# Kernel tuning notes

Measured on AMD Instinct MI355X. Metric: run time of the kernel, lower is better.

## Reference

```python
import jax, jax.numpy as jnp
import numpy as np

N, D, H = 8192, 1024, 256

def setup_inputs() -> dict:
    key = jax.random.key(0)
    ks = jax.random.split(key, 11)
    s = lambda fan_in: 1.0 / np.sqrt(fan_in)
    return {
        "x": jax.random.normal(ks[0], (N, D), dtype=jnp.float32),
        "lin1_w": jax.random.uniform(ks[1], (H, D), jnp.float32, -s(D), s(D)),
        "lin1_b": jax.random.uniform(ks[2], (H,), jnp.float32, -s(D), s(D)),
        "q_w": jax.random.uniform(ks[3], (H, H), jnp.float32, -s(H), s(H)),
        "q_b": jax.random.uniform(ks[4], (H,), jnp.float32, -s(H), s(H)),
        "k_w": jax.random.uniform(ks[5], (H, H), jnp.float32, -s(H), s(H)),
        "k_b": jax.random.uniform(ks[6], (H,), jnp.float32, -s(H), s(H)),
        "v_w": jax.random.uniform(ks[7], (H, H), jnp.float32, -s(H), s(H)),
        "v_b": jax.random.uniform(ks[8], (H,), jnp.float32, -s(H), s(H)),
        "lin2_w": jax.random.uniform(ks[9], (1, H), jnp.float32, -s(H), s(H)),
        "lin2_b": jax.random.uniform(ks[10], (1,), jnp.float32, -s(H), s(H)),
    }

def reference(x, lin1_w, lin1_b, q_w, q_b, k_w, k_b, v_w, v_b, lin2_w, lin2_b):
    h = x @ lin1_w.T + lin1_b                      # [N, H]
    q = h @ q_w.T + q_b                            # [N, H]
    k = h @ k_w.T + k_b                            # [N, H]
    v = h @ v_w.T + v_b                            # [N, H]
    scale = 1.0 / np.sqrt(H).astype(np.float32)
    w = (q @ k.T) * scale                          # [N, N] dense scores
    a = jax.nn.softmax(w, axis=-1)                 # row softmax
    h = h + a @ v                                  # residual
    out = h @ lin2_w.T + lin2_b                    # [N, 1]
    return out.squeeze(-1)                         # [N]
```

## Files before the change

### kernel.cpp

```cpp
#include <hip/hip_runtime.h>
#include <hip/hip_bf16.h>
#include <math.h>

typedef __attribute__((ext_vector_type(4))) float f32x4;
typedef __attribute__((ext_vector_type(8))) short bf16x8;

#define N_TOK 8192
#define D_IN  1024
#define H_DIM 256
#define S_SPLIT 16
#define QSCALE 0.09016844f

static __device__ __forceinline__ float bf2f(unsigned short u) {
  return __uint_as_float(((unsigned)u) << 16);
}
static __device__ __forceinline__ float fast_exp2(float x) {
  float e;
  asm("v_exp_f32 %0, %1" : "=v"(e) : "v"(x));
  return e;
}
static __device__ __forceinline__ void gload_lds16(const void* g, void* l) {
  __builtin_amdgcn_global_load_lds(
      (const __attribute__((address_space(1))) void*)g,
      (__attribute__((address_space(3))) void*)l, 16, 0, 0);
}

__global__ __launch_bounds__(256) void prep_kernel(
    const float* __restrict__ w1, const float* __restrict__ qw,
    const float* __restrict__ kw, const float* __restrict__ vw,
    const float* __restrict__ vb, const float* __restrict__ w2,
    __hip_bfloat16* __restrict__ w1b, __hip_bfloat16* __restrict__ qwb,
    __hip_bfloat16* __restrict__ kwb, float* __restrict__ wv2, float* __restrict__ bv2)
{
  int b = blockIdx.x, tid = threadIdx.x;
  if (b < 384) {
    const float* in; __hip_bfloat16* out; int base;
    if (b < 256)      { in = w1; out = w1b; base = b; }
    else if (b < 320) { in = qw; out = qwb; base = b - 256; }
    else              { in = kw; out = kwb; base = b - 320; }
    int i = base * 1024 + tid * 4;
    float4 v = *reinterpret_cast<const float4*>(in + i);
    union { __hip_bfloat16 h[4]; ushort4 u; } cv;
    cv.h[0] = __float2bfloat16(v.x);
    cv.h[1] = __float2bfloat16(v.y);
    cv.h[2] = __float2bfloat16(v.z);
    cv.h[3] = __float2bfloat16(v.w);
    *reinterpret_cast<ushort4*>(out + i) = cv.u;
    return;
  }
  __shared__ float sw2[256];
  __shared__ float red[256];
  sw2[tid] = w2[tid];
  __syncthreads();
  float a = 0.f;
  #pragma unroll 8
  for (int c = 0; c < 256; ++c) a += vw[c * 256 + tid] * sw2[c];
  wv2[tid] = a;
  red[tid] = vb[tid] * sw2[tid];
  __syncthreads();
  for (int s = 128; s > 0; s >>= 1) {
    if (tid < s) red[tid] += red[tid + s];
    __syncthreads();
  }
  if (tid == 0) bv2[0] = red[0];
}

__global__ __launch_bounds__(512, 4) void lin1_kernel(
    const float* __restrict__ x, const __hip_bfloat16* __restrict__ W1,
    const float* __restrict__ b1, __hip_bfloat16* __restrict__ Ho)
{
  __shared__ __attribute__((aligned(16))) unsigned char lds[2][20480];
  const int tid = threadIdx.x;
  const int w = tid >> 6, l = tid & 63, r16 = l & 15, kg = l >> 4;
  const int wr = w >> 2, wc = w & 3;
  const int rowbase = blockIdx.x * 32;
  const int ch = blockIdx.y;
  const char* Wb = (const char*)W1 + (size_t)ch * 128 * 2048;

  const int xrow = tid >> 4;
  const int xc   = tid & 15;
  const float* xsrc = x + (size_t)(rowbase + xrow) * D_IN + xc * 4;
  const int xdst = xrow * 128 + ((xc * 8) ^ ((xrow & 7) << 4));

  f32x4 acc[2];
  acc[0] = (f32x4){0.f, 0.f, 0.f, 0.f};
  acc[1] = (f32x4){0.f, 0.f, 0.f, 0.f};

  {
    f32x4 xv = *reinterpret_cast<const f32x4*>(xsrc);
    #pragma unroll
    for (int i = 0; i < 2; ++i) {
      int p = i * 8192 + tid * 16;
      int col = p >> 7, bb = p & 127;
      gload_lds16(Wb + (size_t)col * 2048 + (bb ^ ((col & 7) << 4)), &lds[0][4096 + p]);
    }
    union { __hip_bfloat16 h[4]; ushort4 u; } cv;
    cv.h[0] = __float2bfloat16(xv[0]); cv.h[1] = __float2bfloat16(xv[1]);
    cv.h[2] = __float2bfloat16(xv[2]); cv.h[3] = __float2bfloat16(xv[3]);
    *reinterpret_cast<ushort4*>(&lds[0][xdst]) = cv.u;
  }
  __syncthreads();

  const int rsw = (r16 & 7) << 4;
  for (int t = 0; t < 16; ++t) {
    const int cur = t & 1;
    f32x4 xv;
    if (t + 1 < 16) {
      xv = *reinterpret_cast<const f32x4*>(xsrc + (t + 1) * 64);
      const int k0b = (t + 1) * 128;
      #pragma unroll
      for (int i = 0; i < 2; ++i) {
        int p = i * 8192 + tid * 16;
        int col = p >> 7, bb = p & 127;
        gload_lds16(Wb + (size_t)col * 2048 + k0b + (bb ^ ((col & 7) << 4)),
                    &lds[cur ^ 1][4096 + p]);
      }
    }
    const unsigned char* A = &lds[cur][0];
    const unsigned char* W = &lds[cur][4096];
    #pragma unroll
    for (int ks = 0; ks < 2; ++ks) {
      bf16x8 a = *reinterpret_cast<const bf16x8*>(
          A + (wr * 16 + r16) * 128 + ((ks * 64 + kg * 16) ^ rsw));
      #pragma unroll
      for (int c = 0; c < 2; ++c) {
        const int colloc = wc * 32 + c * 16 + r16;
        bf16x8 b = *reinterpret_cast<const bf16x8*>(
            W + colloc * 128 + ((ks * 64 + kg * 16) ^ rsw));
        acc[c] = __builtin_amdgcn_mfma_f32_16x16x32_bf16(a, b, acc[c], 0, 0, 0);
      }
    }
    if (t + 1 < 16) {
      union { __hip_bfloat16 h[4]; ushort4 u; } cv;
      cv.h[0] = __float2bfloat16(xv[0]); cv.h[1] = __float2bfloat16(xv[1]);
      cv.h[2] = __float2bfloat16(xv[2]); cv.h[3] = __float2bfloat16(xv[3]);
      *reinterpret_cast<ushort4*>(&lds[cur ^ 1][xdst]) = cv.u;
    }
    __syncthreads();
  }

  #pragma unroll
  for (int c = 0; c < 2; ++c) {
    int colloc = wc * 32 + c * 16 + r16;
    float bs = b1[ch * 128 + colloc];
    #pragma unroll
    for (int j = 0; j < 4; ++j)
      *reinterpret_cast<__hip_bfloat16*>(
          &lds[0][(wr * 16 + kg * 4 + j) * 256 + colloc * 2]) =
          __float2bfloat16(acc[c][j] + bs);
  }
  __syncthreads();
  {
    int row = tid >> 4, byteo = (tid & 15) * 16;
    uint4 v = *reinterpret_cast<uint4*>(&lds[0][row * 256 + byteo]);
    *reinterpret_cast<uint4*>((char*)Ho + (size_t)(rowbase + row) * 512 + ch * 256 + byteo) = v;
  }
}

__global__ __launch_bounds__(256, 3) void qk_kernel(
    const __hip_bfloat16* __restrict__ Hi,
    const __hip_bfloat16* __restrict__ Wq, const __hip_bfloat16* __restrict__ Wk,
    const float* __restrict__ bq, const float* __restrict__ bk,
    const float* __restrict__ w2, const float* __restrict__ wv2, const float* __restrict__ b2,
    __hip_bfloat16* __restrict__ Qo, __hip_bfloat16* __restrict__ Ko,
    float* __restrict__ hw2, float* __restrict__ vs)
{
  __shared__ __attribute__((aligned(16))) unsigned char lds[8192 + 4096];
  const int tid = threadIdx.x;
  const int w = tid >> 6, l = tid & 63, r16 = l & 15, kg = l >> 4;
  const int rowbase = blockIdx.x * 16;
  const bool isq = (blockIdx.y & 2) == 0;
  const int ch = blockIdx.y & 1;
  const __hip_bfloat16* Wp = isq ? Wq : Wk;
  const int colloc_base = w * 32;
  const int colg_base = ch * 128 + colloc_base;

  #pragma unroll
  for (int i = 0; i < 2; ++i) {
    int p = i * 4096 + tid * 16;
    int row = p >> 9, bb = p & 511;
    gload_lds16((const char*)Hi + (size_t)(rowbase + row) * 512 + (bb ^ ((row & 7) << 4)),
                &lds[p]);
  }

  bf16x8 bfr[8][2];
  #pragma unroll
  for (int ks = 0; ks < 8; ++ks)
    #pragma unroll
    for (int c = 0; c < 2; ++c)
      bfr[ks][c] = *reinterpret_cast<const bf16x8*>(
          Wp + (size_t)(colg_base + c * 16 + r16) * H_DIM + ks * 32 + kg * 8);

  __syncthreads();

  const int rsw = (r16 & 7) << 4;
  bf16x8 afr[8];
  #pragma unroll
  for (int ks = 0; ks < 8; ++ks)
    afr[ks] = *reinterpret_cast<const bf16x8*>(
        &lds[0] + r16 * 512 + ((ks * 64 + kg * 16) ^ rsw));

  f32x4 acc[2];
  acc[0] = (f32x4){0.f, 0.f, 0.f, 0.f};
  acc[1] = (f32x4){0.f, 0.f, 0.f, 0.f};
  #pragma unroll
  for (int ks = 0; ks < 8; ++ks)
    #pragma unroll
    for (int c = 0; c < 2; ++c)
      acc[c] = __builtin_amdgcn_mfma_f32_16x16x32_bf16(afr[ks], bfr[ks][c], acc[c], 0, 0, 0);

  const float* bp = isq ? bq : bk;
  const float scl = isq ? QSCALE : 1.f;
  #pragma unroll
  for (int c = 0; c < 2; ++c) {
    int colloc = colloc_base + c * 16 + r16;
    float bb = bp[ch * 128 + colloc];
    #pragma unroll
    for (int j = 0; j < 4; ++j)
      *reinterpret_cast<__hip_bfloat16*>(&lds[8192 + (kg * 4 + j) * 256 + colloc * 2]) =
          __float2bfloat16((acc[c][j] + bb) * scl);
  }
  __syncthreads();
  {
    int row = tid >> 4, byteo = (tid & 15) * 16;
    uint4 v = *reinterpret_cast<const uint4*>(&lds[8192 + row * 256 + byteo]);
    char* dst = (char*)(isq ? Qo : Ko) + (size_t)(rowbase + row) * 512 + ch * 256 + byteo;
    *reinterpret_cast<uint4*>(dst) = v;
  }
  if (ch == 0) {
    const float* wsel = isq ? w2 : wv2;
    int row = w * 4 + (l >> 4);
    int c16 = l & 15;
    int rs2 = (row & 7) << 4;
    bf16x8 h0 = *reinterpret_cast<const bf16x8*>(&lds[0] + row * 512 + ((c16 * 32) ^ rs2));
    bf16x8 h1 = *reinterpret_cast<const bf16x8*>(&lds[0] + row * 512 + ((c16 * 32 + 16) ^ rs2));
    float s = 0.f;
    #pragma unroll
    for (int i = 0; i < 8; ++i) s += bf2f((unsigned short)h0[i]) * wsel[c16 * 16 + i];
    #pragma unroll
    for (int i = 0; i < 8; ++i) s += bf2f((unsigned short)h1[i]) * wsel[c16 * 16 + 8 + i];
    #pragma unroll
    for (int off = 1; off < 16; off <<= 1) s += __shfl_xor(s, off);
    if (c16 == 0) {
      if (isq) hw2[rowbase + row] = s + b2[0];
      else     vs[rowbase + row]  = s;
    }
  }
}

#define KVBLK 64
#define KRANGE (N_TOK / S_SPLIT)
__global__ __launch_bounds__(256, 2) void attn_partial_kernel(
    const __hip_bfloat16* __restrict__ Q, const __hip_bfloat16* __restrict__ K,
    const float* __restrict__ vsg, float* __restrict__ pden, float* __restrict__ pacc)
{
  __shared__ __attribute__((aligned(16))) unsigned char ktile[2][KVBLK * 512];
  __shared__ float vs_lds[KRANGE];

  const int tid = threadIdx.x;
  const int w   = tid >> 6;
  const int l   = tid & 63;
  const int r16 = l & 15;
  const int kg  = l >> 4;
  const int split   = blockIdx.y;
  const int mstart  = split * KRANGE;
  const int rowbase = blockIdx.x * 256 + w * 64;

  if (tid < KRANGE / 4)
    *reinterpret_cast<float4*>(vs_lds + tid * 4) =
        *reinterpret_cast<const float4*>(vsg + mstart + tid * 4);

  bf16x8 qf[4][8];
  #pragma unroll
  for (int sub = 0; sub < 4; ++sub) {
    const __hip_bfloat16* qp = Q + (size_t)(rowbase + sub * 16 + r16) * H_DIM + kg * 8;
    #pragma unroll
    for (int kk = 0; kk < 8; ++kk) qf[sub][kk] = *reinterpret_cast<const bf16x8*>(qp + kk * 32);
  }

  const int trow = tid >> 5;
  const int tbsw = ((tid & 31) * 16) ^ ((trow & 7) << 4);
  const char* kbase = (const char*)K + (size_t)(mstart + trow) * 512 + tbsw;
  const int ldst = trow * 512 + (tid & 31) * 16;

  const int rsw = (r16 & 7) << 4;
  const int cb  = kg * 16;

  float den[4][4], acc[4][4];
  #pragma unroll
  for (int sub = 0; sub < 4; ++sub)
    #pragma unroll
    for (int j = 0; j < 4; ++j) { den[sub][j] = 0.f; acc[sub][j] = 0.f; }

  #pragma unroll
  for (int i = 0; i < 8; ++i)
    gload_lds16(kbase + (size_t)(i * 8) * 512, &ktile[0][i * 4096 + ldst]);
  __syncthreads();

  const int NT = KRANGE / KVBLK;
  for (int t = 0; t < NT; ++t) {
    const int cur = t & 1;
    if (t + 1 < NT) {
      #pragma unroll
      for (int i = 0; i < 8; ++i)
        gload_lds16(kbase + (size_t)((t + 1) * KVBLK + i * 8) * 512,
                    &ktile[cur ^ 1][i * 4096 + ldst]);
    }

    const unsigned char* kt = &ktile[cur][0];
    #pragma unroll
    for (int h = 0; h < 2; ++h) {
      f32x4 d[4][2];
      #pragma unroll
      for (int sub = 0; sub < 4; ++sub)
        #pragma unroll
        for (int n = 0; n < 2; ++n) d[sub][n] = (f32x4){0.f, 0.f, 0.f, 0.f};

      __builtin_amdgcn_s_setprio(1);
      #pragma unroll
      for (int n = 0; n < 2; ++n) {
        const int row = h * 32 + n * 16 + r16;
        #pragma unroll
        for (int kk = 0; kk < 8; ++kk) {
          bf16x8 b = *reinterpret_cast<const bf16x8*>(
              kt + row * 512 + ((kk * 64 + cb) ^ rsw));
          d[0][n] = __builtin_amdgcn_mfma_f32_16x16x32_bf16(qf[0][kk], b, d[0][n], 0, 0, 0);
          d[1][n] = __builtin_amdgcn_mfma_f32_16x16x32_bf16(qf[1][kk], b, d[1][n], 0, 0, 0);
          d[2][n] = __builtin_amdgcn_mfma_f32_16x16x32_bf16(qf[2][kk], b, d[2][n], 0, 0, 0);
          d[3][n] = __builtin_amdgcn_mfma_f32_16x16x32_bf16(qf[3][kk], b, d[3][n], 0, 0, 0);
        }
      }
      __builtin_amdgcn_s_setprio(0);

      const float vsm0 = vs_lds[t * KVBLK + h * 32 + r16];
      const float vsm1 = vs_lds[t * KVBLK + h * 32 + 16 + r16];
      #pragma unroll
      for (int sub = 0; sub < 4; ++sub)
        #pragma unroll
        for (int j = 0; j < 4; ++j) {
          float e0 = fast_exp2(d[sub][0][j]);
          float e1 = fast_exp2(d[sub][1][j]);
          den[sub][j] += e0 + e1;
          acc[sub][j] = fmaf(e0, vsm0, fmaf(e1, vsm1, acc[sub][j]));
        }
    }
    __syncthreads();
  }

  #pragma unroll
  for (int sub = 0; sub < 4; ++sub)
    #pragma unroll
    for (int j = 0; j < 4; ++j) {
      #pragma unroll
      for (int off = 1; off < 16; off <<= 1) {
        den[sub][j] += __shfl_xor(den[sub][j], off);
        acc[sub][j] += __shfl_xor(acc[sub][j], off);
      }
    }
  if (r16 == 0) {
    #pragma unroll
    for (int sub = 0; sub < 4; ++sub)
      #pragma unroll
      for (int j = 0; j < 4; ++j) {
        int row = rowbase + sub * 16 + kg * 4 + j;
        pden[split * N_TOK + row] = den[sub][j];
        pacc[split * N_TOK + row] = acc[sub][j];
      }
  }
}

__global__ __launch_bounds__(256) void combine_kernel(
    const float* __restrict__ pden, const float* __restrict__ pacc,
    const float* __restrict__ hw2, const float* __restrict__ bv2, float* __restrict__ out)
{
  int r = blockIdx.x * 256 + threadIdx.x;
  float den = 0.f, acc = 0.f;
  #pragma unroll
  for (int s = 0; s < S_SPLIT; ++s) {
    den += pden[s * N_TOK + r];
    acc += pacc[s * N_TOK + r];
  }
  out[r] = hw2[r] + acc / den + bv2[0];
}

extern "C" void kernel_launch(void* const* d_in, const int* in_sizes, int n_in,
                              void* d_out, int out_size, void* d_ws, size_t ws_size,
                              hipStream_t stream) {
  const float* x      = (const float*)d_in[0];
  const float* lin1_w = (const float*)d_in[1];
  const float* lin1_b = (const float*)d_in[2];
  const float* q_w    = (const float*)d_in[3];
  const float* q_b    = (const float*)d_in[4];
  const float* k_w    = (const float*)d_in[5];
  const float* k_b    = (const float*)d_in[6];
  const float* v_w    = (const float*)d_in[7];
  const float* v_b    = (const float*)d_in[8];
  const float* lin2_w = (const float*)d_in[9];
  const float* lin2_b = (const float*)d_in[10];
  float* out = (float*)d_out;

  char* ws = (char*)d_ws;
  size_t off = 0;
  auto alloc = [&](size_t bytes) {
    char* p = ws + off;
    off += (bytes + 255) & ~(size_t)255;
    return p;
  };
  __hip_bfloat16* w1b = (__hip_bfloat16*)alloc((size_t)H_DIM * D_IN * 2);
  __hip_bfloat16* qwb = (__hip_bfloat16*)alloc((size_t)H_DIM * H_DIM * 2);
  __hip_bfloat16* kwb = (__hip_bfloat16*)alloc((size_t)H_DIM * H_DIM * 2);
  __hip_bfloat16* hb  = (__hip_bfloat16*)alloc((size_t)N_TOK * H_DIM * 2);
  __hip_bfloat16* qb  = (__hip_bfloat16*)alloc((size_t)N_TOK * H_DIM * 2);
  __hip_bfloat16* kb  = (__hip_bfloat16*)alloc((size_t)N_TOK * H_DIM * 2);
  float* hw2  = (float*)alloc((size_t)N_TOK * 4);
  float* vsv  = (float*)alloc((size_t)N_TOK * 4);
  float* wv2  = (float*)alloc((size_t)H_DIM * 4);
  float* bv2  = (float*)alloc(256);
  float* pden = (float*)alloc((size_t)S_SPLIT * N_TOK * 4);
  float* pacc = (float*)alloc((size_t)S_SPLIT * N_TOK * 4);
  (void)ws_size; (void)in_sizes; (void)n_in; (void)out_size;

  prep_kernel<<<385, 256, 0, stream>>>(lin1_w, q_w, k_w, v_w, v_b, lin2_w,
                                       w1b, qwb, kwb, wv2, bv2);

  lin1_kernel<<<dim3(N_TOK / 32, 2), 512, 0, stream>>>(x, w1b, lin1_b, hb);

  qk_kernel<<<dim3(N_TOK / 16, 4), 256, 0, stream>>>(hb, qwb, kwb, q_b, k_b,
                                                     lin2_w, wv2, lin2_b, qb, kb, hw2, vsv);

  attn_partial_kernel<<<dim3(32, S_SPLIT), 256, 0, stream>>>(qb, kb, vsv, pden, pacc);

  combine_kernel<<<N_TOK / 256, 256, 0, stream>>>(pden, pacc, hw2, bv2, out);
}
```

Before: 93.96 us.

## Give each wave its own K tile pipeline and stage v_w through LDS

```diff
diff --git a/kernel.cpp b/kernel.cpp
--- a/kernel.cpp
+++ b/kernel.cpp
@@ -49,20 +49,31 @@
     return;
   }
   __shared__ float sw2[256];
-  __shared__ float red[256];
+  __shared__ __attribute__((aligned(16))) float vch[32 * 256];
   sw2[tid] = w2[tid];
-  __syncthreads();
   float a = 0.f;
-  #pragma unroll 8
-  for (int c = 0; c < 256; ++c) a += vw[c * 256 + tid] * sw2[c];
+  for (int ch = 0; ch < 8; ++ch) {
+    __syncthreads();
+    #pragma unroll
+    for (int i = 0; i < 8; ++i) {
+      int p = i * 1024 + tid * 4;
+      *reinterpret_cast<float4*>(vch + p) =
+          *reinterpret_cast<const float4*>(vw + ch * 8192 + p);
+    }
+    __syncthreads();
+    #pragma unroll
+    for (int c = 0; c < 32; ++c)
+      a = fmaf(vch[c * 256 + tid], sw2[ch * 32 + c], a);
+  }
   wv2[tid] = a;
-  red[tid] = vb[tid] * sw2[tid];
+  __syncthreads();
+  vch[tid] = vb[tid] * sw2[tid];
   __syncthreads();
   for (int s = 128; s > 0; s >>= 1) {
-    if (tid < s) red[tid] += red[tid + s];
+    if (tid < s) vch[tid] += vch[tid + s];
     __syncthreads();
   }
-  if (tid == 0) bv2[0] = red[0];
+  if (tid == 0) bv2[0] = vch[0];
 }
 
 __global__ __launch_bounds__(512, 4) void lin1_kernel(
@@ -248,13 +259,14 @@
   }
 }
 
-#define KVBLK 64
+#define KVW 16
 #define KRANGE (N_TOK / S_SPLIT)
+#define NTW (KRANGE / KVW)
 __global__ __launch_bounds__(256, 2) void attn_partial_kernel(
     const __hip_bfloat16* __restrict__ Q, const __hip_bfloat16* __restrict__ K,
     const float* __restrict__ vsg, float* __restrict__ pden, float* __restrict__ pacc)
 {
-  __shared__ __attribute__((aligned(16))) unsigned char ktile[2][KVBLK * 512];
+  __shared__ __attribute__((aligned(16))) unsigned char ktile[4][2][KVW * 512];
   __shared__ float vs_lds[KRANGE];
 
   const int tid = threadIdx.x;
@@ -278,10 +290,11 @@
     for (int kk = 0; kk < 8; ++kk) qf[sub][kk] = *reinterpret_cast<const bf16x8*>(qp + kk * 32);
   }
 
-  const int trow = tid >> 5;
-  const int tbsw = ((tid & 31) * 16) ^ ((trow & 7) << 4);
-  const char* kbase = (const char*)K + (size_t)(mstart + trow) * 512 + tbsw;
-  const int ldst = trow * 512 + (tid & 31) * 16;
+  const int trow = l >> 5;
+  const int tcol = (l & 31) * 16;
+  const char* kb = (const char*)K + (size_t)mstart * 512;
+  unsigned char* wb0 = &ktile[w][0][0];
+  unsigned char* wb1 = &ktile[w][1][0];
 
   const int rsw = (r16 & 7) << 4;
   const int cb  = kg * 16;
@@ -293,58 +306,52 @@
     for (int j = 0; j < 4; ++j) { den[sub][j] = 0.f; acc[sub][j] = 0.f; }
 
   #pragma unroll
-  for (int i = 0; i < 8; ++i)
-    gload_lds16(kbase + (size_t)(i * 8) * 512, &ktile[0][i * 4096 + ldst]);
-  __syncthreads();
-
-  const int NT = KRANGE / KVBLK;
-  for (int t = 0; t < NT; ++t) {
-    const int cur = t & 1;
-    if (t + 1 < NT) {
-      #pragma unroll
-      for (int i = 0; i < 8; ++i)
-        gload_lds16(kbase + (size_t)((t + 1) * KVBLK + i * 8) * 512,
-                    &ktile[cur ^ 1][i * 4096 + ldst]);
-    }
-
-    const unsigned char* kt = &ktile[cur][0];
-    #pragma unroll
-    for (int h = 0; h < 2; ++h) {
-      f32x4 d[4][2];
-      #pragma unroll
-      for (int sub = 0; sub < 4; ++sub)
-        #pragma unroll
-        for (int n = 0; n < 2; ++n) d[sub][n] = (f32x4){0.f, 0.f, 0.f, 0.f};
-
-      __builtin_amdgcn_s_setprio(1);
-      #pragma unroll
-      for (int n = 0; n < 2; ++n) {
-        const int row = h * 32 + n * 16 + r16;
-        #pragma unroll
-        for (int kk = 0; kk < 8; ++kk) {
-          bf16x8 b = *reinterpret_cast<const bf16x8*>(
-              kt + row * 512 + ((kk * 64 + cb) ^ rsw));
-          d[0][n] = __builtin_amdgcn_mfma_f32_16x16x32_bf16(qf[0][kk], b, d[0][n], 0, 0, 0);
-          d[1][n] = __builtin_amdgcn_mfma_f32_16x16x32_bf16(qf[1][kk], b, d[1][n], 0, 0, 0);
-          d[2][n] = __builtin_amdgcn_mfma_f32_16x16x32_bf16(qf[2][kk], b, d[2][n], 0, 0, 0);
-          d[3][n] = __builtin_amdgcn_mfma_f32_16x16x32_bf16(qf[3][kk], b, d[3][n], 0, 0, 0);
-        }
-      }
-      __builtin_amdgcn_s_setprio(0);
-
-      const float vsm0 = vs_lds[t * KVBLK + h * 32 + r16];
-      const float vsm1 = vs_lds[t * KVBLK + h * 32 + 16 + r16];
-      #pragma unroll
-      for (int sub = 0; sub < 4; ++sub)
-        #pragma unroll
-        for (int j = 0; j < 4; ++j) {
-          float e0 = fast_exp2(d[sub][0][j]);
-          float e1 = fast_exp2(d[sub][1][j]);
-          den[sub][j] += e0 + e1;
-          acc[sub][j] = fmaf(e0, vsm0, fmaf(e1, vsm1, acc[sub][j]));
-        }
-    }
-    __syncthreads();
+  for (int i = 0; i < 8; ++i) {
+    const int rg = i * 2 + trow;
+    gload_lds16(kb + (size_t)rg * 512 + (tcol ^ ((rg & 7) << 4)), wb0 + i * 1024);
+  }
+  __syncthreads();
+
+  for (int t = 0; t < NTW; ++t) {
+    unsigned char* rb = (t & 1) ? wb1 : wb0;
+    unsigned char* pb = (t & 1) ? wb0 : wb1;
+    if (t + 1 < NTW) {
+      const char* kt1 = kb + (size_t)(t + 1) * (KVW * 512);
+      #pragma unroll
+      for (int i = 0; i < 8; ++i) {
+        const int rg = i * 2 + trow;
+        gload_lds16(kt1 + (size_t)rg * 512 + (tcol ^ ((rg & 7) << 4)), pb + i * 1024);
+      }
+      asm volatile("s_waitcnt vmcnt(8)" ::: "memory");
+    } else {
+      asm volatile("s_waitcnt vmcnt(0)" ::: "memory");
+    }
+    __builtin_amdgcn_sched_barrier(0);
+
+    f32x4 d[4];
+    #pragma unroll
+    for (int sub = 0; sub < 4; ++sub) d[sub] = (f32x4){0.f, 0.f, 0.f, 0.f};
+
+    __builtin_amdgcn_s_setprio(1);
+    #pragma unroll
+    for (int kk = 0; kk < 8; ++kk) {
+      bf16x8 b = *reinterpret_cast<const bf16x8*>(rb + r16 * 512 + ((kk * 64 + cb) ^ rsw));
+      d[0] = __builtin_amdgcn_mfma_f32_16x16x32_bf16(qf[0][kk], b, d[0], 0, 0, 0);
+      d[1] = __builtin_amdgcn_mfma_f32_16x16x32_bf16(qf[1][kk], b, d[1], 0, 0, 0);
+      d[2] = __builtin_amdgcn_mfma_f32_16x16x32_bf16(qf[2][kk], b, d[2], 0, 0, 0);
+      d[3] = __builtin_amdgcn_mfma_f32_16x16x32_bf16(qf[3][kk], b, d[3], 0, 0, 0);
+    }
+    __builtin_amdgcn_s_setprio(0);
+
+    const float vsm = vs_lds[t * KVW + r16];
+    #pragma unroll
+    for (int sub = 0; sub < 4; ++sub)
+      #pragma unroll
+      for (int j = 0; j < 4; ++j) {
+        float e = fast_exp2(d[sub][j]);
+        den[sub][j] += e;
+        acc[sub][j] = fmaf(e, vsm, acc[sub][j]);
+      }
   }
 
   #pragma unroll
```

Result: no change. 92.22 us (-1.8%).

## Shrink attention tiles, double grid, use explicit waitcnt barriers; stage v_w in LDS

Applied to the files above, without the earlier changes.

```diff
diff --git a/kernel.cpp b/kernel.cpp
--- a/kernel.cpp
+++ b/kernel.cpp
@@ -49,20 +49,31 @@
     return;
   }
   __shared__ float sw2[256];
-  __shared__ float red[256];
+  __shared__ __attribute__((aligned(16))) float vch[32 * 256];
   sw2[tid] = w2[tid];
-  __syncthreads();
   float a = 0.f;
-  #pragma unroll 8
-  for (int c = 0; c < 256; ++c) a += vw[c * 256 + tid] * sw2[c];
+  for (int ch = 0; ch < 8; ++ch) {
+    __syncthreads();
+    #pragma unroll
+    for (int i = 0; i < 8; ++i) {
+      int p = i * 1024 + tid * 4;
+      *reinterpret_cast<float4*>(vch + p) =
+          *reinterpret_cast<const float4*>(vw + ch * 8192 + p);
+    }
+    __syncthreads();
+    #pragma unroll
+    for (int c = 0; c < 32; ++c)
+      a = fmaf(vch[c * 256 + tid], sw2[ch * 32 + c], a);
+  }
   wv2[tid] = a;
-  red[tid] = vb[tid] * sw2[tid];
+  __syncthreads();
+  vch[tid] = vb[tid] * sw2[tid];
   __syncthreads();
   for (int s = 128; s > 0; s >>= 1) {
-    if (tid < s) red[tid] += red[tid + s];
+    if (tid < s) vch[tid] += vch[tid + s];
     __syncthreads();
   }
-  if (tid == 0) bv2[0] = red[0];
+  if (tid == 0) bv2[0] = vch[0];
 }
 
 __global__ __launch_bounds__(512, 4) void lin1_kernel(
@@ -248,9 +259,10 @@
   }
 }
 
-#define KVBLK 64
+#define KVBLK 32
 #define KRANGE (N_TOK / S_SPLIT)
-__global__ __launch_bounds__(256, 2) void attn_partial_kernel(
+#define NT (KRANGE / KVBLK)
+__global__ __launch_bounds__(256, 3) void attn_partial_kernel(
     const __hip_bfloat16* __restrict__ Q, const __hip_bfloat16* __restrict__ K,
     const float* __restrict__ vsg, float* __restrict__ pden, float* __restrict__ pacc)
 {
@@ -264,91 +276,95 @@
   const int kg  = l >> 4;
   const int split   = blockIdx.y;
   const int mstart  = split * KRANGE;
-  const int rowbase = blockIdx.x * 256 + w * 64;
+  const int rowbase = blockIdx.x * 128 + w * 32;
 
   if (tid < KRANGE / 4)
     *reinterpret_cast<float4*>(vs_lds + tid * 4) =
         *reinterpret_cast<const float4*>(vsg + mstart + tid * 4);
 
-  bf16x8 qf[4][8];
-  #pragma unroll
-  for (int sub = 0; sub < 4; ++sub) {
+  bf16x8 qf[2][8];
+  #pragma unroll
+  for (int sub = 0; sub < 2; ++sub) {
     const __hip_bfloat16* qp = Q + (size_t)(rowbase + sub * 16 + r16) * H_DIM + kg * 8;
     #pragma unroll
     for (int kk = 0; kk < 8; ++kk) qf[sub][kk] = *reinterpret_cast<const bf16x8*>(qp + kk * 32);
   }
 
-  const int trow = tid >> 5;
-  const int tbsw = ((tid & 31) * 16) ^ ((trow & 7) << 4);
-  const char* kbase = (const char*)K + (size_t)(mstart + trow) * 512 + tbsw;
-  const int ldst = trow * 512 + (tid & 31) * 16;
+  const char* kb = (const char*)K + (size_t)mstart * 512;
+  int soff[4];
+  #pragma unroll
+  for (int i = 0; i < 4; ++i) {
+    int p = i * 4096 + tid * 16;
+    int row = p >> 9, bb = p & 511;
+    soff[i] = row * 512 + (bb ^ ((row & 7) << 4));
+  }
 
   const int rsw = (r16 & 7) << 4;
   const int cb  = kg * 16;
 
-  float den[4][4], acc[4][4];
-  #pragma unroll
-  for (int sub = 0; sub < 4; ++sub)
+  float den[2][4], acc[2][4];
+  #pragma unroll
+  for (int sub = 0; sub < 2; ++sub)
     #pragma unroll
     for (int j = 0; j < 4; ++j) { den[sub][j] = 0.f; acc[sub][j] = 0.f; }
 
   #pragma unroll
-  for (int i = 0; i < 8; ++i)
-    gload_lds16(kbase + (size_t)(i * 8) * 512, &ktile[0][i * 4096 + ldst]);
-  __syncthreads();
-
-  const int NT = KRANGE / KVBLK;
+  for (int i = 0; i < 4; ++i)
+    gload_lds16(kb + soff[i], &ktile[0][i * 4096 + tid * 16]);
+  __syncthreads();
+
   for (int t = 0; t < NT; ++t) {
     const int cur = t & 1;
     if (t + 1 < NT) {
-      #pragma unroll
-      for (int i = 0; i < 8; ++i)
-        gload_lds16(kbase + (size_t)((t + 1) * KVBLK + i * 8) * 512,
-                    &ktile[cur ^ 1][i * 4096 + ldst]);
-    }
+      const char* kt1 = kb + (size_t)(t + 1) * (KVBLK * 512);
+      #pragma unroll
+      for (int i = 0; i < 4; ++i)
+        gload_lds16(kt1 + soff[i], &ktile[cur ^ 1][i * 4096 + tid * 16]);
+      asm volatile("s_waitcnt vmcnt(4)" ::: "memory");
+    } else {
+      asm volatile("s_waitcnt vmcnt(0)" ::: "memory");
+    }
+    __builtin_amdgcn_s_barrier();
+    __builtin_amdgcn_sched_barrier(0);
 
     const unsigned char* kt = &ktile[cur][0];
-    #pragma unroll
-    for (int h = 0; h < 2; ++h) {
-      f32x4 d[4][2];
-      #pragma unroll
-      for (int sub = 0; sub < 4; ++sub)
-        #pragma unroll
-        for (int n = 0; n < 2; ++n) d[sub][n] = (f32x4){0.f, 0.f, 0.f, 0.f};
-
-      __builtin_amdgcn_s_setprio(1);
-      #pragma unroll
-      for (int n = 0; n < 2; ++n) {
-        const int row = h * 32 + n * 16 + r16;
-        #pragma unroll
-        for (int kk = 0; kk < 8; ++kk) {
-          bf16x8 b = *reinterpret_cast<const bf16x8*>(
-              kt + row * 512 + ((kk * 64 + cb) ^ rsw));
-          d[0][n] = __builtin_amdgcn_mfma_f32_16x16x32_bf16(qf[0][kk], b, d[0][n], 0, 0, 0);
-          d[1][n] = __builtin_amdgcn_mfma_f32_16x16x32_bf16(qf[1][kk], b, d[1][n], 0, 0, 0);
-          d[2][n] = __builtin_amdgcn_mfma_f32_16x16x32_bf16(qf[2][kk], b, d[2][n], 0, 0, 0);
-          d[3][n] = __builtin_amdgcn_mfma_f32_16x16x32_bf16(qf[3][kk], b, d[3][n], 0, 0, 0);
-        }
-      }
-      __builtin_amdgcn_s_setprio(0);
-
-      const float vsm0 = vs_lds[t * KVBLK + h * 32 + r16];
-      const float vsm1 = vs_lds[t * KVBLK + h * 32 + 16 + r16];
-      #pragma unroll
-      for (int sub = 0; sub < 4; ++sub)
-        #pragma unroll
-        for (int j = 0; j < 4; ++j) {
-          float e0 = fast_exp2(d[sub][0][j]);
-          float e1 = fast_exp2(d[sub][1][j]);
-          den[sub][j] += e0 + e1;
-          acc[sub][j] = fmaf(e0, vsm0, fmaf(e1, vsm1, acc[sub][j]));
-        }
-    }
-    __syncthreads();
-  }
-
-  #pragma unroll
-  for (int sub = 0; sub < 4; ++sub)
+    f32x4 d[2][2];
+    #pragma unroll
+    for (int sub = 0; sub < 2; ++sub)
+      #pragma unroll
+      for (int n = 0; n < 2; ++n) d[sub][n] = (f32x4){0.f, 0.f, 0.f, 0.f};
+
+    __builtin_amdgcn_s_setprio(1);
+    #pragma unroll
+    for (int n = 0; n < 2; ++n) {
+      #pragma unroll
+      for (int kk = 0; kk < 8; ++kk) {
+        bf16x8 b = *reinterpret_cast<const bf16x8*>(
+            kt + (n * 16 + r16) * 512 + ((kk * 64 + cb) ^ rsw));
+        d[0][n] = __builtin_amdgcn_mfma_f32_16x16x32_bf16(qf[0][kk], b, d[0][n], 0, 0, 0);
+        d[1][n] = __builtin_amdgcn_mfma_f32_16x16x32_bf16(qf[1][kk], b, d[1][n], 0, 0, 0);
+      }
+    }
+    __builtin_amdgcn_s_setprio(0);
+
+    const float vsm0 = vs_lds[t * KVBLK + r16];
+    const float vsm1 = vs_lds[t * KVBLK + 16 + r16];
+    #pragma unroll
+    for (int sub = 0; sub < 2; ++sub)
+      #pragma unroll
+      for (int j = 0; j < 4; ++j) {
+        float e0 = fast_exp2(d[sub][0][j]);
+        float e1 = fast_exp2(d[sub][1][j]);
+        den[sub][j] += e0 + e1;
+        acc[sub][j] = fmaf(e0, vsm0, fmaf(e1, vsm1, acc[sub][j]));
+      }
+
+    __builtin_amdgcn_sched_barrier(0);
+    __builtin_amdgcn_s_barrier();
+  }
+
+  #pragma unroll
+  for (int sub = 0; sub < 2; ++sub)
     #pragma unroll
     for (int j = 0; j < 4; ++j) {
       #pragma unroll
@@ -359,7 +375,7 @@
     }
   if (r16 == 0) {
     #pragma unroll
-    for (int sub = 0; sub < 4; ++sub)
+    for (int sub = 0; sub < 2; ++sub)
       #pragma unroll
       for (int j = 0; j < 4; ++j) {
         int row = rowbase + sub * 16 + kg * 4 + j;
@@ -428,7 +444,7 @@
   qk_kernel<<<dim3(N_TOK / 16, 4), 256, 0, stream>>>(hb, qwb, kwb, q_b, k_b,
                                                      lin2_w, wv2, lin2_b, qb, kb, hw2, vsv);
 
-  attn_partial_kernel<<<dim3(32, S_SPLIT), 256, 0, stream>>>(qb, kb, vsv, pden, pacc);
+  attn_partial_kernel<<<dim3(64, S_SPLIT), 256, 0, stream>>>(qb, kb, vsv, pden, pacc);
 
   combine_kernel<<<N_TOK / 256, 256, 0, stream>>>(pden, pacc, hw2, bv2, out);
 }
```

After: 99.48 us. 1.06x slower.

## Fuse lin1 and Q/K projection into one front kernel keeping h in LDS

Applied to the files above, without the earlier changes.

```diff
diff --git a/kernel.cpp b/kernel.cpp
--- a/kernel.cpp
+++ b/kernel.cpp
@@ -49,59 +49,73 @@
     return;
   }
   __shared__ float sw2[256];
-  __shared__ float red[256];
+  __shared__ __attribute__((aligned(16))) float vch[32 * 256];
   sw2[tid] = w2[tid];
+  float a = 0.f;
+  for (int ch = 0; ch < 8; ++ch) {
+    __syncthreads();
+    #pragma unroll
+    for (int i = 0; i < 8; ++i) {
+      int p = i * 1024 + tid * 4;
+      *reinterpret_cast<float4*>(vch + p) =
+          *reinterpret_cast<const float4*>(vw + ch * 8192 + p);
+    }
+    __syncthreads();
+    #pragma unroll
+    for (int c = 0; c < 32; ++c)
+      a = fmaf(vch[c * 256 + tid], sw2[ch * 32 + c], a);
+  }
+  wv2[tid] = a;
   __syncthreads();
-  float a = 0.f;
-  #pragma unroll 8
-  for (int c = 0; c < 256; ++c) a += vw[c * 256 + tid] * sw2[c];
-  wv2[tid] = a;
-  red[tid] = vb[tid] * sw2[tid];
+  vch[tid] = vb[tid] * sw2[tid];
   __syncthreads();
   for (int s = 128; s > 0; s >>= 1) {
-    if (tid < s) red[tid] += red[tid + s];
-    __syncthreads();
-  }
-  if (tid == 0) bv2[0] = red[0];
-}
-
-__global__ __launch_bounds__(512, 4) void lin1_kernel(
+    if (tid < s) vch[tid] += vch[tid + s];
+    __syncthreads();
+  }
+  if (tid == 0) bv2[0] = vch[0];
+}
+
+__global__ __launch_bounds__(512) void front_kernel(
     const float* __restrict__ x, const __hip_bfloat16* __restrict__ W1,
-    const float* __restrict__ b1, __hip_bfloat16* __restrict__ Ho)
+    const __hip_bfloat16* __restrict__ Wq, const __hip_bfloat16* __restrict__ Wk,
+    const float* __restrict__ b1, const float* __restrict__ bq, const float* __restrict__ bk,
+    const float* __restrict__ w2, const float* __restrict__ wv2, const float* __restrict__ b2,
+    __hip_bfloat16* __restrict__ Qo, __hip_bfloat16* __restrict__ Ko,
+    float* __restrict__ hw2, float* __restrict__ vs)
 {
-  __shared__ __attribute__((aligned(16))) unsigned char lds[2][20480];
+  __shared__ __attribute__((aligned(16))) unsigned char h_lds[16384];
+  __shared__ __attribute__((aligned(16))) unsigned char sbuf[2][36864];
   const int tid = threadIdx.x;
   const int w = tid >> 6, l = tid & 63, r16 = l & 15, kg = l >> 4;
   const int wr = w >> 2, wc = w & 3;
   const int rowbase = blockIdx.x * 32;
-  const int ch = blockIdx.y;
-  const char* Wb = (const char*)W1 + (size_t)ch * 128 * 2048;
-
-  const int xrow = tid >> 4;
-  const int xc   = tid & 15;
+  const int rsw = (r16 & 7) << 4;
+
+  const int xrow = tid >> 4, xc = tid & 15;
   const float* xsrc = x + (size_t)(rowbase + xrow) * D_IN + xc * 4;
   const int xdst = xrow * 128 + ((xc * 8) ^ ((xrow & 7) << 4));
-
-  f32x4 acc[2];
-  acc[0] = (f32x4){0.f, 0.f, 0.f, 0.f};
-  acc[1] = (f32x4){0.f, 0.f, 0.f, 0.f};
+  const char* W1b = (const char*)W1;
+
+  f32x4 acc[4];
+  #pragma unroll
+  for (int c = 0; c < 4; ++c) acc[c] = (f32x4){0.f, 0.f, 0.f, 0.f};
 
   {
     f32x4 xv = *reinterpret_cast<const f32x4*>(xsrc);
     #pragma unroll
-    for (int i = 0; i < 2; ++i) {
+    for (int i = 0; i < 4; ++i) {
       int p = i * 8192 + tid * 16;
       int col = p >> 7, bb = p & 127;
-      gload_lds16(Wb + (size_t)col * 2048 + (bb ^ ((col & 7) << 4)), &lds[0][4096 + p]);
+      gload_lds16(W1b + (size_t)col * 2048 + (bb ^ ((col & 7) << 4)), &sbuf[0][4096 + p]);
     }
     union { __hip_bfloat16 h[4]; ushort4 u; } cv;
     cv.h[0] = __float2bfloat16(xv[0]); cv.h[1] = __float2bfloat16(xv[1]);
     cv.h[2] = __float2bfloat16(xv[2]); cv.h[3] = __float2bfloat16(xv[3]);
-    *reinterpret_cast<ushort4*>(&lds[0][xdst]) = cv.u;
+    *reinterpret_cast<ushort4*>(&sbuf[0][xdst]) = cv.u;
   }
   __syncthreads();
 
-  const int rsw = (r16 & 7) << 4;
   for (int t = 0; t < 16; ++t) {
     const int cur = t & 1;
     f32x4 xv;
@@ -109,22 +123,22 @@
       xv = *reinterpret_cast<const f32x4*>(xsrc + (t + 1) * 64);
       const int k0b = (t + 1) * 128;
       #pragma unroll
-      for (int i = 0; i < 2; ++i) {
+      for (int i = 0; i < 4; ++i) {
         int p = i * 8192 + tid * 16;
         int col = p >> 7, bb = p & 127;
-        gload_lds16(Wb + (size_t)col * 2048 + k0b + (bb ^ ((col & 7) << 4)),
-                    &lds[cur ^ 1][4096 + p]);
-      }
-    }
-    const unsigned char* A = &lds[cur][0];
-    const unsigned char* W = &lds[cur][4096];
+        gload_lds16(W1b + (size_t)col * 2048 + k0b + (bb ^ ((col & 7) << 4)),
+                    &sbuf[cur ^ 1][4096 + p]);
+      }
+    }
+    const unsigned char* A = &sbuf[cur][0];
+    const unsigned char* W = &sbuf[cur][4096];
     #pragma unroll
     for (int ks = 0; ks < 2; ++ks) {
       bf16x8 a = *reinterpret_cast<const bf16x8*>(
           A + (wr * 16 + r16) * 128 + ((ks * 64 + kg * 16) ^ rsw));
       #pragma unroll
-      for (int c = 0; c < 2; ++c) {
-        const int colloc = wc * 32 + c * 16 + r16;
+      for (int c = 0; c < 4; ++c) {
+        const int colloc = wc * 64 + c * 16 + r16;
         bf16x8 b = *reinterpret_cast<const bf16x8*>(
             W + colloc * 128 + ((ks * 64 + kg * 16) ^ rsw));
         acc[c] = __builtin_amdgcn_mfma_f32_16x16x32_bf16(a, b, acc[c], 0, 0, 0);
@@ -134,116 +148,112 @@
       union { __hip_bfloat16 h[4]; ushort4 u; } cv;
       cv.h[0] = __float2bfloat16(xv[0]); cv.h[1] = __float2bfloat16(xv[1]);
       cv.h[2] = __float2bfloat16(xv[2]); cv.h[3] = __float2bfloat16(xv[3]);
-      *reinterpret_cast<ushort4*>(&lds[cur ^ 1][xdst]) = cv.u;
-    }
-    __syncthreads();
-  }
-
-  #pragma unroll
-  for (int c = 0; c < 2; ++c) {
-    int colloc = wc * 32 + c * 16 + r16;
-    float bs = b1[ch * 128 + colloc];
-    #pragma unroll
-    for (int j = 0; j < 4; ++j)
+      *reinterpret_cast<ushort4*>(&sbuf[cur ^ 1][xdst]) = cv.u;
+    }
+    __syncthreads();
+  }
+
+  #pragma unroll
+  for (int c = 0; c < 4; ++c) {
+    int col = wc * 64 + c * 16 + r16;
+    float bs = b1[col];
+    #pragma unroll
+    for (int j = 0; j < 4; ++j) {
+      int row = wr * 16 + kg * 4 + j;
       *reinterpret_cast<__hip_bfloat16*>(
-          &lds[0][(wr * 16 + kg * 4 + j) * 256 + colloc * 2]) =
+          &h_lds[row * 512 + ((col * 2) ^ ((row & 7) << 4))]) =
           __float2bfloat16(acc[c][j] + bs);
+    }
+  }
+
+  const char* wqB = (const char*)Wq;
+  const char* wkB = (const char*)Wk;
+  #pragma unroll
+  for (int i = 0; i < 4; ++i) {
+    int p = i * 8192 + tid * 16;
+    int col = p >> 7, bb = p & 127;
+    gload_lds16(wqB + (size_t)col * 512 + (bb ^ ((col & 7) << 4)), &sbuf[0][p]);
   }
   __syncthreads();
+
+  f32x4 qacc[4];
+  #pragma unroll
+  for (int c = 0; c < 4; ++c) qacc[c] = (f32x4){0.f, 0.f, 0.f, 0.f};
+
+  for (int r = 0; r < 8; ++r) {
+    const int buf = r & 1;
+    if (r + 1 < 8) {
+      const char* Wsel = (r + 1 < 4) ? wqB : wkB;
+      const int kq1 = (r + 1) & 3;
+      #pragma unroll
+      for (int i = 0; i < 4; ++i) {
+        int p = i * 8192 + tid * 16;
+        int col = p >> 7, bb = p & 127;
+        gload_lds16(Wsel + (size_t)col * 512 + kq1 * 128 + (bb ^ ((col & 7) << 4)),
+                    &sbuf[buf ^ 1][p]);
+      }
+    }
+    const int kq = r & 3;
+    const unsigned char* WT = &sbuf[buf][0];
+    #pragma unroll
+    for (int ks = 0; ks < 2; ++ks) {
+      bf16x8 a = *reinterpret_cast<const bf16x8*>(
+          &h_lds[(wr * 16 + r16) * 512 + ((kq * 128 + ks * 64 + kg * 16) ^ rsw)]);
+      #pragma unroll
+      for (int c = 0; c < 4; ++c) {
+        const int colloc = wc * 64 + c * 16 + r16;
+        bf16x8 b = *reinterpret_cast<const bf16x8*>(
+            WT + colloc * 128 + ((ks * 64 + kg * 16) ^ rsw));
+        qacc[c] = __builtin_amdgcn_mfma_f32_16x16x32_bf16(a, b, qacc[c], 0, 0, 0);
+      }
+    }
+    if (r == 3) {
+      #pragma unroll
+      for (int c = 0; c < 4; ++c) {
+        int col = wc * 64 + c * 16 + r16;
+        float bb = bq[col];
+        #pragma unroll
+        for (int j = 0; j < 4; ++j) {
+          int row = rowbase + wr * 16 + kg * 4 + j;
+          Qo[(size_t)row * H_DIM + col] = __float2bfloat16((qacc[c][j] + bb) * QSCALE);
+        }
+        qacc[c] = (f32x4){0.f, 0.f, 0.f, 0.f};
+      }
+    }
+    __syncthreads();
+  }
+  #pragma unroll
+  for (int c = 0; c < 4; ++c) {
+    int col = wc * 64 + c * 16 + r16;
+    float bb = bk[col];
+    #pragma unroll
+    for (int j = 0; j < 4; ++j) {
+      int row = rowbase + wr * 16 + kg * 4 + j;
+      Ko[(size_t)row * H_DIM + col] = __float2bfloat16(qacc[c][j] + bb);
+    }
+  }
+
   {
-    int row = tid >> 4, byteo = (tid & 15) * 16;
-    uint4 v = *reinterpret_cast<uint4*>(&lds[0][row * 256 + byteo]);
-    *reinterpret_cast<uint4*>((char*)Ho + (size_t)(rowbase + row) * 512 + ch * 256 + byteo) = v;
-  }
-}
-
-__global__ __launch_bounds__(256, 3) void qk_kernel(
-    const __hip_bfloat16* __restrict__ Hi,
-    const __hip_bfloat16* __restrict__ Wq, const __hip_bfloat16* __restrict__ Wk,
-    const float* __restrict__ bq, const float* __restrict__ bk,
-    const float* __restrict__ w2, const float* __restrict__ wv2, const float* __restrict__ b2,
-    __hip_bfloat16* __restrict__ Qo, __hip_bfloat16* __restrict__ Ko,
-    float* __restrict__ hw2, float* __restrict__ vs)
-{
-  __shared__ __attribute__((aligned(16))) unsigned char lds[8192 + 4096];
-  const int tid = threadIdx.x;
-  const int w = tid >> 6, l = tid & 63, r16 = l & 15, kg = l >> 4;
-  const int rowbase = blockIdx.x * 16;
-  const bool isq = (blockIdx.y & 2) == 0;
-  const int ch = blockIdx.y & 1;
-  const __hip_bfloat16* Wp = isq ? Wq : Wk;
-  const int colloc_base = w * 32;
-  const int colg_base = ch * 128 + colloc_base;
-
-  #pragma unroll
-  for (int i = 0; i < 2; ++i) {
-    int p = i * 4096 + tid * 16;
-    int row = p >> 9, bb = p & 511;
-    gload_lds16((const char*)Hi + (size_t)(rowbase + row) * 512 + (bb ^ ((row & 7) << 4)),
-                &lds[p]);
-  }
-
-  bf16x8 bfr[8][2];
-  #pragma unroll
-  for (int ks = 0; ks < 8; ++ks)
-    #pragma unroll
-    for (int c = 0; c < 2; ++c)
-      bfr[ks][c] = *reinterpret_cast<const bf16x8*>(
-          Wp + (size_t)(colg_base + c * 16 + r16) * H_DIM + ks * 32 + kg * 8);
-
-  __syncthreads();
-
-  const int rsw = (r16 & 7) << 4;
-  bf16x8 afr[8];
-  #pragma unroll
-  for (int ks = 0; ks < 8; ++ks)
-    afr[ks] = *reinterpret_cast<const bf16x8*>(
-        &lds[0] + r16 * 512 + ((ks * 64 + kg * 16) ^ rsw));
-
-  f32x4 acc[2];
-  acc[0] = (f32x4){0.f, 0.f, 0.f, 0.f};
-  acc[1] = (f32x4){0.f, 0.f, 0.f, 0.f};
-  #pragma unroll
-  for (int ks = 0; ks < 8; ++ks)
-    #pragma unroll
-    for (int c = 0; c < 2; ++c)
-      acc[c] = __builtin_amdgcn_mfma_f32_16x16x32_bf16(afr[ks], bfr[ks][c], acc[c], 0, 0, 0);
-
-  const float* bp = isq ? bq : bk;
-  const float scl = isq ? QSCALE : 1.f;
-  #pragma unroll
-  for (int c = 0; c < 2; ++c) {
-    int colloc = colloc_base + c * 16 + r16;
-    float bb = bp[ch * 128 + colloc];
-    #pragma unroll
-    for (int j = 0; j < 4; ++j)
-      *reinterpret_cast<__hip_bfloat16*>(&lds[8192 + (kg * 4 + j) * 256 + colloc * 2]) =
-          __float2bfloat16((acc[c][j] + bb) * scl);
-  }
-  __syncthreads();
-  {
-    int row = tid >> 4, byteo = (tid & 15) * 16;
-    uint4 v = *reinterpret_cast<const uint4*>(&lds[8192 + row * 256 + byteo]);
-    char* dst = (char*)(isq ? Qo : Ko) + (size_t)(rowbase + row) * 512 + ch * 256 + byteo;
-    *reinterpret_cast<uint4*>(dst) = v;
-  }
-  if (ch == 0) {
-    const float* wsel = isq ? w2 : wv2;
-    int row = w * 4 + (l >> 4);
-    int c16 = l & 15;
-    int rs2 = (row & 7) << 4;
-    bf16x8 h0 = *reinterpret_cast<const bf16x8*>(&lds[0] + row * 512 + ((c16 * 32) ^ rs2));
-    bf16x8 h1 = *reinterpret_cast<const bf16x8*>(&lds[0] + row * 512 + ((c16 * 32 + 16) ^ rs2));
-    float s = 0.f;
-    #pragma unroll
-    for (int i = 0; i < 8; ++i) s += bf2f((unsigned short)h0[i]) * wsel[c16 * 16 + i];
-    #pragma unroll
-    for (int i = 0; i < 8; ++i) s += bf2f((unsigned short)h1[i]) * wsel[c16 * 16 + 8 + i];
-    #pragma unroll
-    for (int off = 1; off < 16; off <<= 1) s += __shfl_xor(s, off);
-    if (c16 == 0) {
-      if (isq) hw2[rowbase + row] = s + b2[0];
-      else     vs[rowbase + row]  = s;
+    const bool isw2 = (w < 4);
+    const float* wsel = isw2 ? w2 : wv2;
+    const int c16 = l & 15;
+    #pragma unroll
+    for (int pass = 0; pass < 2; ++pass) {
+      int row = (w & 3) * 8 + pass * 4 + (l >> 4);
+      int rs2 = (row & 7) << 4;
+      bf16x8 h0 = *reinterpret_cast<const bf16x8*>(&h_lds[row * 512 + ((c16 * 32) ^ rs2)]);
+      bf16x8 h1 = *reinterpret_cast<const bf16x8*>(&h_lds[row * 512 + ((c16 * 32 + 16) ^ rs2)]);
+      float s = 0.f;
+      #pragma unroll
+      for (int i = 0; i < 8; ++i) s += bf2f((unsigned short)h0[i]) * wsel[c16 * 16 + i];
+      #pragma unroll
+      for (int i = 0; i < 8; ++i) s += bf2f((unsigned short)h1[i]) * wsel[c16 * 16 + 8 + i];
+      #pragma unroll
+      for (int off = 1; off < 16; off <<= 1) s += __shfl_xor(s, off);
+      if (c16 == 0) {
+        if (isw2) hw2[rowbase + row] = s + b2[0];
+        else      vs[rowbase + row]  = s;
+      }
     }
   }
 }
@@ -409,7 +419,6 @@
   __hip_bfloat16* w1b = (__hip_bfloat16*)alloc((size_t)H_DIM * D_IN * 2);
   __hip_bfloat16* qwb = (__hip_bfloat16*)alloc((size_t)H_DIM * H_DIM * 2);
   __hip_bfloat16* kwb = (__hip_bfloat16*)alloc((size_t)H_DIM * H_DIM * 2);
-  __hip_bfloat16* hb  = (__hip_bfloat16*)alloc((size_t)N_TOK * H_DIM * 2);
   __hip_bfloat16* qb  = (__hip_bfloat16*)alloc((size_t)N_TOK * H_DIM * 2);
   __hip_bfloat16* kb  = (__hip_bfloat16*)alloc((size_t)N_TOK * H_DIM * 2);
   float* hw2  = (float*)alloc((size_t)N_TOK * 4);
@@ -423,10 +432,8 @@
   prep_kernel<<<385, 256, 0, stream>>>(lin1_w, q_w, k_w, v_w, v_b, lin2_w,
                                        w1b, qwb, kwb, wv2, bv2);
 
-  lin1_kernel<<<dim3(N_TOK / 32, 2), 512, 0, stream>>>(x, w1b, lin1_b, hb);
-
-  qk_kernel<<<dim3(N_TOK / 16, 4), 256, 0, stream>>>(hb, qwb, kwb, q_b, k_b,
-                                                     lin2_w, wv2, lin2_b, qb, kb, hw2, vsv);
+  front_kernel<<<256, 512, 0, stream>>>(x, w1b, qwb, kwb, lin1_b, q_b, k_b,
+                                        lin2_w, wv2, lin2_b, qb, kb, hw2, vsv);
 
   attn_partial_kernel<<<dim3(32, S_SPLIT), 256, 0, stream>>>(qb, kb, vsv, pden, pacc);
 
```

After: 81.39 us. -13.4%, faster.
